# Optimization experiments

Measured on AMD Instinct MI355X. Metric: run time of the kernel, lower is better.

## Reference

```python
import jax, jax.numpy as jnp
import numpy as np


def log_g(x):
    # log(relu(x) + 0.5) for x >= 0, else -softplus(-x)
    pos = jnp.log(jnp.maximum(x, 0.0) + 0.5)
    neg = -jax.nn.softplus(-x)
    return jnp.where(x >= 0, pos, neg)


def parallel_scan_log(log_coeffs, log_values):
    # h_t = a_t * h_{t-1} + b_t, computed stably in log space
    a_star = jnp.cumsum(log_coeffs, axis=1)
    log_h0_plus_b_star = jax.lax.cumlogsumexp(log_values - a_star, axis=1)
    log_h = a_star + log_h0_plus_b_star
    return jnp.exp(log_h)


def setup_inputs() -> dict:
    key = jax.random.key(0)
    k1, k2 = jax.random.split(key)
    B, S, D = 8, 4096, 1024
    x = jax.random.normal(k1, (B, S, D), dtype=jnp.float32)
    # torch nn.Linear(dim, 2*inner_dim, bias=False): weight [2*inner_dim, dim]
    W_hg = jax.random.normal(k2, (2 * D, D), dtype=jnp.float32) * (1.0 / np.sqrt(D))
    return {"x": x, "W_hg": W_hg}


def reference(x, W_hg):
    # hidden_gate projection: [B,S,D] @ [D, 2*inner] -> [B,S,2*inner]
    hg = jnp.einsum("bsd,ed->bse", x, W_hg)
    hidden, gate = jnp.split(hg, 2, axis=-1)
    log_coeffs = -jax.nn.softplus(gate)       # log(1 - z)
    log_z = -jax.nn.softplus(-gate)           # log(z)
    log_tilde_h = log_g(hidden)
    log_values = log_z + log_tilde_h
    out = parallel_scan_log(log_coeffs, log_values)
    # expansion_factor == 1.0 -> self.out is Identity; dropout_prob == 0 -> Identity
    return out
```

## Files before the change

### kernel.cpp

```cpp
#include <hip/hip_runtime.h>

#define B_   8
#define S_   4096
#define D_   1024
#define M_   (B_ * S_)
#define N_   (2 * D_)
#define K_   D_
#define CCH  128
#define LCH  32

#define BK   32
#define NT   (K_ / BK)

typedef __attribute__((ext_vector_type(8))) short bf16x8;
typedef __attribute__((ext_vector_type(4))) float f32x4;

__device__ __forceinline__ unsigned short f2bf(float f) {
  union { float f; unsigned u; } v; v.f = f;
  unsigned u = v.u;
  u = u + 0x7fffu + ((u >> 16) & 1u);
  return (unsigned short)(u >> 16);
}
__device__ __forceinline__ float bf2f(unsigned short h) {
  union { unsigned u; float f; } v; v.u = ((unsigned)h) << 16;
  return v.f;
}
__device__ __forceinline__ float sigmoidf_(float x) {
  return 1.0f / (1.0f + __expf(-x));
}

#define GLL(src, dst) __builtin_amdgcn_global_load_lds(                     \
      (const __attribute__((address_space(1))) void*)(src),                 \
      (__attribute__((address_space(3))) void*)(dst), 16, 0, 0)

__global__ __launch_bounds__(256) void k_cvt2(const float* __restrict__ x,
                                              const float* __restrict__ W,
                                              unsigned short* __restrict__ xb,
                                              unsigned short* __restrict__ wb) {
  const int n4x = (M_ * K_) / 4;
  const int n4t = n4x + (N_ * K_) / 4;
  int i = blockIdx.x * 256 + threadIdx.x;
  const int stride = gridDim.x * 256;
  for (; i < n4t; i += stride) {
    const float4* src = (i < n4x) ? &reinterpret_cast<const float4*>(x)[i]
                                  : &reinterpret_cast<const float4*>(W)[i - n4x];
    float4 v = *src;
    ushort4 o;
    o.x = f2bf(v.x); o.y = f2bf(v.y); o.z = f2bf(v.z); o.w = f2bf(v.w);
    if (i < n4x) reinterpret_cast<ushort4*>(xb)[i] = o;
    else         reinterpret_cast<ushort4*>(wb)[i - n4x] = o;
  }
}

__global__ __launch_bounds__(256, 3) void k_gemm(const unsigned short* __restrict__ xb,
                                                 const unsigned short* __restrict__ wb,
                                                 unsigned short* __restrict__ Gp,
                                                 unsigned short* __restrict__ Zp) {
  __shared__ unsigned short lds[24576];
  const int tid = threadIdx.x;
  int wg = blockIdx.x;
  wg = (wg & 7) * 512 + (wg >> 3);
  const int bm = wg >> 4;
  const int bn = wg & 15;
  const int lane = tid & 63;
  const int wid = tid >> 6;
  const int wr = wid >> 1;
  const int wc = wid & 1;
  const int fr = lane & 15;
  const int hi = lane >> 4;

  const int srow = tid >> 2;
  const int scol = ((tid & 3) ^ ((srow >> 1) & 3)) * 16;
  const char* aS = (const char*)xb + (size_t)(bm * 128 + srow) * 2048 + scol;
  const char* bS = (const char*)wb + (size_t)(bn * 128 + srow) * 2048 + scol;
  char* const ldsc = (char*)lds + (size_t)tid * 16;
  const char* const ldsr = (const char*)lds;

  const int sA = ((hi ^ ((fr >> 1) & 3)) * 16);
  const int arow = (wr * 64 + fr) * 64;
  const int brow = (wc * 64 + fr) * 64;

  f32x4 acc[4][4] = {};
  bf16x8 av[4], bv[4];

  GLL(aS,          ldsc);          GLL(aS + 131072,      ldsc + 4096);
  GLL(bS,          ldsc + 8192);   GLL(bS + 131072,      ldsc + 12288);
  GLL(aS + 64,     ldsc + 16384);  GLL(aS + 131072 + 64, ldsc + 20480);
  GLL(bS + 64,     ldsc + 24576);  GLL(bS + 131072 + 64, ldsc + 28672);
  asm volatile("s_waitcnt vmcnt(4)\n\ts_barrier" ::: "memory");

  int sl = 0;
  int sn = 32768;

  for (int t = 0; t < NT; ++t) {
    const bool st2 = (t < NT - 2);
    if (st2) {
      const size_t kb = (size_t)(t + 2) * 64;
      char* dq = ldsc + sn;
      GLL(aS + kb,          dq);          GLL(aS + 131072 + kb, dq + 4096);
      GLL(bS + kb,          dq + 8192);   GLL(bS + 131072 + kb, dq + 12288);
    }
    const char* Ab = ldsr + sl;
    const char* Bb = Ab + 8192;
#pragma unroll
    for (int m = 0; m < 4; ++m)
      av[m] = *(const bf16x8*)(Ab + arow + m * 1024 + sA);
#pragma unroll
    for (int n = 0; n < 4; ++n)
      bv[n] = *(const bf16x8*)(Bb + brow + n * 1024 + sA);
    __builtin_amdgcn_s_setprio(1);
#pragma unroll
    for (int m = 0; m < 4; ++m)
#pragma unroll
      for (int n = 0; n < 4; ++n)
        acc[m][n] = __builtin_amdgcn_mfma_f32_16x16x32_bf16(av[m], bv[n], acc[m][n], 0, 0, 0);
    __builtin_amdgcn_s_setprio(0);
    if (st2) asm volatile("s_waitcnt vmcnt(4)\n\ts_barrier" ::: "memory");
    else     asm volatile("s_waitcnt vmcnt(0)\n\ts_barrier" ::: "memory");
    sl += 16384; if (sl == 49152) sl = 0;
    sn += 16384; if (sn == 49152) sn = 0;
  }

  const int row0 = bm * 128 + wr * 64 + (hi << 2);
  const int col0 = bn * 128 + wc * 64 + fr;
  if (bn < 8) {
#pragma unroll
    for (int m = 0; m < 4; ++m)
#pragma unroll
      for (int n = 0; n < 4; ++n)
#pragma unroll
        for (int i = 0; i < 4; ++i) {
          float v = acc[m][n][i];
          float g = (v >= 0.0f) ? (v + 0.5f) : sigmoidf_(v);
          Gp[(size_t)(row0 + m * 16 + i) * 1024 + (col0 + n * 16)] = f2bf(g);
        }
  } else {
#pragma unroll
    for (int m = 0; m < 4; ++m)
#pragma unroll
      for (int n = 0; n < 4; ++n)
#pragma unroll
        for (int i = 0; i < 4; ++i) {
          float v = acc[m][n][i];
          Zp[(size_t)(row0 + m * 16 + i) * 1024 + (col0 + n * 16 - 1024)] = f2bf(sigmoidf_(v));
        }
  }
}

__global__ __launch_bounds__(256) void k_scan1(const unsigned short* __restrict__ Gp,
                                               const unsigned short* __restrict__ Zp,
                                               float* __restrict__ Ap,
                                               float* __restrict__ Hp) {
  const int gid = blockIdx.x * 256 + threadIdx.x;
  const int c = blockIdx.y;
  const int b = gid >> 8;
  const int d0 = (gid & 255) << 2;
  size_t base = ((size_t)b * S_ + (size_t)c * LCH) * 1024 + d0;
  float4 aP = {1.f, 1.f, 1.f, 1.f};
  float4 h  = {0.f, 0.f, 0.f, 0.f};
#pragma unroll 8
  for (int s = 0; s < LCH; ++s) {
    ushort4 zu = *reinterpret_cast<const ushort4*>(Zp + base);
    ushort4 gu = *reinterpret_cast<const ushort4*>(Gp + base);
    float z0 = bf2f(zu.x), z1 = bf2f(zu.y), z2 = bf2f(zu.z), z3 = bf2f(zu.w);
    float a0 = 1.f - z0,   a1 = 1.f - z1,   a2 = 1.f - z2,   a3 = 1.f - z3;
    h.x = fmaf(a0, h.x, z0 * bf2f(gu.x));
    h.y = fmaf(a1, h.y, z1 * bf2f(gu.y));
    h.z = fmaf(a2, h.z, z2 * bf2f(gu.z));
    h.w = fmaf(a3, h.w, z3 * bf2f(gu.w));
    aP.x *= a0; aP.y *= a1; aP.z *= a2; aP.w *= a3;
    base += 1024;
  }
  reinterpret_cast<float4*>(Ap)[(size_t)c * 2048 + gid] = aP;
  reinterpret_cast<float4*>(Hp)[(size_t)c * 2048 + gid] = h;
}

__global__ __launch_bounds__(256) void k_scan2(const float* __restrict__ Ap,
                                               const float* __restrict__ Hp,
                                               float* __restrict__ Cin) {
  const int gid = blockIdx.x * 256 + threadIdx.x;
  float4 carry = {0.f, 0.f, 0.f, 0.f};
  for (int c = 0; c < CCH; ++c) {
    reinterpret_cast<float4*>(Cin)[(size_t)c * 2048 + gid] = carry;
    float4 a = reinterpret_cast<const float4*>(Ap)[(size_t)c * 2048 + gid];
    float4 hh = reinterpret_cast<const float4*>(Hp)[(size_t)c * 2048 + gid];
    carry.x = fmaf(a.x, carry.x, hh.x);
    carry.y = fmaf(a.y, carry.y, hh.y);
    carry.z = fmaf(a.z, carry.z, hh.z);
    carry.w = fmaf(a.w, carry.w, hh.w);
  }
}

__global__ __launch_bounds__(256) void k_scan3(const unsigned short* __restrict__ Gp,
                                               const unsigned short* __restrict__ Zp,
                                               const float* __restrict__ Cin,
                                               float* __restrict__ out) {
  const int gid = blockIdx.x * 256 + threadIdx.x;
  const int c = blockIdx.y;
  const int b = gid >> 8;
  const int d0 = (gid & 255) << 2;
  size_t base = ((size_t)b * S_ + (size_t)c * LCH) * 1024 + d0;
  float4 h = reinterpret_cast<const float4*>(Cin)[(size_t)c * 2048 + gid];
#pragma unroll 8
  for (int s = 0; s < LCH; ++s) {
    ushort4 zu = *reinterpret_cast<const ushort4*>(Zp + base);
    ushort4 gu = *reinterpret_cast<const ushort4*>(Gp + base);
    float z0 = bf2f(zu.x), z1 = bf2f(zu.y), z2 = bf2f(zu.z), z3 = bf2f(zu.w);
    h.x = fmaf(1.f - z0, h.x, z0 * bf2f(gu.x));
    h.y = fmaf(1.f - z1, h.y, z1 * bf2f(gu.y));
    h.z = fmaf(1.f - z2, h.z, z2 * bf2f(gu.z));
    h.w = fmaf(1.f - z3, h.w, z3 * bf2f(gu.w));
    *reinterpret_cast<float4*>(out + base) = h;
    base += 1024;
  }
}

extern "C" void kernel_launch(void* const* d_in, const int* in_sizes, int n_in,
                              void* d_out, int out_size, void* d_ws, size_t ws_size,
                              hipStream_t stream) {
  const float* x = (const float*)d_in[0];
  const float* W = (const float*)d_in[1];
  float* out = (float*)d_out;

  unsigned char* w = (unsigned char*)d_ws;
  unsigned short* xb = (unsigned short*)(w);
  unsigned short* wb = (unsigned short*)(w + 67108864);
  unsigned short* Gp = (unsigned short*)(w + 67108864 + 4194304);
  unsigned short* Zp = (unsigned short*)(w + 67108864 + 4194304 + 67108864);
  float* Ap  = (float*)(w);
  float* Hp  = (float*)(w + 4194304);
  float* Cin = (float*)(w + 8388608);

  k_cvt2<<<4096, 256, 0, stream>>>(x, W, xb, wb);
  k_gemm<<<(M_ / 128) * (N_ / 128), 256, 0, stream>>>(xb, wb, Gp, Zp);
  k_scan1<<<dim3(8, CCH), 256, 0, stream>>>(Gp, Zp, Ap, Hp);
  k_scan2<<<8, 256, 0, stream>>>(Ap, Hp, Cin);
  k_scan3<<<dim3(8, CCH), 256, 0, stream>>>(Gp, Zp, Cin, out);
}
```

Measured before the change: 287.6 us.

## Enlarge GEMM block tile to 256x128 with 8 waves sharing B tile

Switches the GEMM workgroup from 256 threads computing a 128x128 tile to 512 threads computing a 256x128 tile. Each B (weight) tile loaded into LDS is now reused by twice as many rows, which cuts global and LDS traffic per output element, and the grid swizzle is adjusted to match. The cost is a larger LDS footprint per block (72KB triple buffer), which may limit how many blocks fit per CU and lowers the total number of workgroups.

After: 273.6 us. 4.9% less time.

```diff
diff --git a/kernel.cpp b/kernel.cpp
--- a/kernel.cpp
+++ b/kernel.cpp
@@ -52,62 +52,64 @@
   }
 }
 
-__global__ __launch_bounds__(256, 3) void k_gemm(const unsigned short* __restrict__ xb,
+__global__ __launch_bounds__(512, 4) void k_gemm(const unsigned short* __restrict__ xb,
                                                  const unsigned short* __restrict__ wb,
                                                  unsigned short* __restrict__ Gp,
                                                  unsigned short* __restrict__ Zp) {
-  __shared__ unsigned short lds[24576];
+  __shared__ unsigned short lds[36864];
   const int tid = threadIdx.x;
   int wg = blockIdx.x;
-  wg = (wg & 7) * 512 + (wg >> 3);
+  wg = (wg & 7) * 256 + (wg >> 3);
   const int bm = wg >> 4;
   const int bn = wg & 15;
   const int lane = tid & 63;
   const int wid = tid >> 6;
-  const int wr = wid >> 1;
-  const int wc = wid & 1;
+  const int wrr = wid >> 1;
+  const int wcc = wid & 1;
   const int fr = lane & 15;
   const int hi = lane >> 4;
 
   const int srow = tid >> 2;
   const int scol = ((tid & 3) ^ ((srow >> 1) & 3)) * 16;
-  const char* aS = (const char*)xb + (size_t)(bm * 128 + srow) * 2048 + scol;
+  const char* aS = (const char*)xb + (size_t)(bm * 256 + srow) * 2048 + scol;
   const char* bS = (const char*)wb + (size_t)(bn * 128 + srow) * 2048 + scol;
   char* const ldsc = (char*)lds + (size_t)tid * 16;
   const char* const ldsr = (const char*)lds;
 
   const int sA = ((hi ^ ((fr >> 1) & 3)) * 16);
-  const int arow = (wr * 64 + fr) * 64;
-  const int brow = (wc * 64 + fr) * 64;
+  const int arow = (wrr * 64 + fr) * 64;
+  const int brow = 16384 + (wcc * 64 + fr) * 64;
 
   f32x4 acc[4][4] = {};
   bf16x8 av[4], bv[4];
 
-  GLL(aS,          ldsc);          GLL(aS + 131072,      ldsc + 4096);
-  GLL(bS,          ldsc + 8192);   GLL(bS + 131072,      ldsc + 12288);
-  GLL(aS + 64,     ldsc + 16384);  GLL(aS + 131072 + 64, ldsc + 20480);
-  GLL(bS + 64,     ldsc + 24576);  GLL(bS + 131072 + 64, ldsc + 28672);
-  asm volatile("s_waitcnt vmcnt(4)\n\ts_barrier" ::: "memory");
+  GLL(aS,               ldsc);
+  GLL(aS + 262144,      ldsc + 8192);
+  GLL(bS,               ldsc + 16384);
+  GLL(aS + 64,          ldsc + 24576);
+  GLL(aS + 262144 + 64, ldsc + 32768);
+  GLL(bS + 64,          ldsc + 40960);
+  asm volatile("s_waitcnt vmcnt(3)\n\ts_barrier" ::: "memory");
 
   int sl = 0;
-  int sn = 32768;
+  int sn = 49152;
 
   for (int t = 0; t < NT; ++t) {
     const bool st2 = (t < NT - 2);
     if (st2) {
       const size_t kb = (size_t)(t + 2) * 64;
       char* dq = ldsc + sn;
-      GLL(aS + kb,          dq);          GLL(aS + 131072 + kb, dq + 4096);
-      GLL(bS + kb,          dq + 8192);   GLL(bS + 131072 + kb, dq + 12288);
+      GLL(aS + kb,               dq);
+      GLL(aS + 262144 + kb,      dq + 8192);
+      GLL(bS + kb,               dq + 16384);
     }
     const char* Ab = ldsr + sl;
-    const char* Bb = Ab + 8192;
 #pragma unroll
     for (int m = 0; m < 4; ++m)
       av[m] = *(const bf16x8*)(Ab + arow + m * 1024 + sA);
 #pragma unroll
     for (int n = 0; n < 4; ++n)
-      bv[n] = *(const bf16x8*)(Bb + brow + n * 1024 + sA);
+      bv[n] = *(const bf16x8*)(Ab + brow + n * 1024 + sA);
     __builtin_amdgcn_s_setprio(1);
 #pragma unroll
     for (int m = 0; m < 4; ++m)
@@ -115,14 +117,14 @@
       for (int n = 0; n < 4; ++n)
         acc[m][n] = __builtin_amdgcn_mfma_f32_16x16x32_bf16(av[m], bv[n], acc[m][n], 0, 0, 0);
     __builtin_amdgcn_s_setprio(0);
-    if (st2) asm volatile("s_waitcnt vmcnt(4)\n\ts_barrier" ::: "memory");
+    if (st2) asm volatile("s_waitcnt vmcnt(3)\n\ts_barrier" ::: "memory");
     else     asm volatile("s_waitcnt vmcnt(0)\n\ts_barrier" ::: "memory");
-    sl += 16384; if (sl == 49152) sl = 0;
-    sn += 16384; if (sn == 49152) sn = 0;
-  }
-
-  const int row0 = bm * 128 + wr * 64 + (hi << 2);
-  const int col0 = bn * 128 + wc * 64 + fr;
+    sl += 24576; if (sl == 73728) sl = 0;
+    sn += 24576; if (sn == 73728) sn = 0;
+  }
+
+  const int row0 = bm * 256 + wrr * 64 + (hi << 2);
+  const int col0 = bn * 128 + wcc * 64 + fr;
   if (bn < 8) {
 #pragma unroll
     for (int m = 0; m < 4; ++m)
@@ -232,7 +234,7 @@
   float* Cin = (float*)(w + 8388608);
 
   k_cvt2<<<4096, 256, 0, stream>>>(x, W, xb, wb);
-  k_gemm<<<(M_ / 128) * (N_ / 128), 256, 0, stream>>>(xb, wb, Gp, Zp);
+  k_gemm<<<(M_ / 256) * (N_ / 128), 512, 0, stream>>>(xb, wb, Gp, Zp);
   k_scan1<<<dim3(8, CCH), 256, 0, stream>>>(Gp, Zp, Ap, Hp);
   k_scan2<<<8, 256, 0, stream>>>(Ap, Hp, Cin);
   k_scan3<<<dim3(8, CCH), 256, 0, stream>>>(Gp, Zp, Cin, out);
```
